# Kernel optimization log

Hardware: AMD Instinct MI355X
Metric: run time of the kernel (lower is better)

Reference implementation:

```python
import jax, jax.numpy as jnp
import numpy as np

HIDDEN = 256
NUM_STEPS = 3
N_NODES = 200000
N_GRAPHS = 512


def setup_inputs() -> dict:
    key = jax.random.key(0)
    ks = jax.random.split(key, 8)
    h = HIDDEN
    x = jax.random.normal(ks[0], (N_NODES, h), dtype=jnp.float32)
    batch = jnp.sort(jax.random.randint(ks[1], (N_NODES,), 0, N_GRAPHS)).astype(jnp.int64)
    s_ih = 1.0 / np.sqrt(2 * h)
    s_hh = 1.0 / np.sqrt(h)
    # LSTM (input 2h -> hidden h), PyTorch gate order i,f,g,o
    W_ih = jax.random.uniform(ks[2], (4 * h, 2 * h), jnp.float32, -s_ih, s_ih)
    W_hh = jax.random.uniform(ks[3], (4 * h, h), jnp.float32, -s_hh, s_hh)
    b_ih = jax.random.uniform(ks[4], (4 * h,), jnp.float32, -s_hh, s_hh)
    b_hh = jax.random.uniform(ks[5], (4 * h,), jnp.float32, -s_hh, s_hh)
    # out_proj: Linear(2h -> h)
    s_o = 1.0 / np.sqrt(2 * h)
    W_out = jax.random.uniform(ks[6], (h, 2 * h), jnp.float32, -s_o, s_o)
    b_out = jax.random.uniform(ks[7], (h,), jnp.float32, -s_o, s_o)
    return {"x": x, "batch": batch, "W_ih": W_ih, "W_hh": W_hh,
            "b_ih": b_ih, "b_hh": b_hh, "W_out": W_out, "b_out": b_out,
            "n_graphs": N_GRAPHS}


def _set2set(x, batch, W_ih, W_hh, b_ih, b_hh, n_graphs):
    h = x.shape[1]
    hs = jnp.zeros((n_graphs, h), x.dtype)
    cs = jnp.zeros((n_graphs, h), x.dtype)
    q_star = jnp.zeros((n_graphs, 2 * h), x.dtype)
    for _ in range(NUM_STEPS):
        # LSTM step (PyTorch gate order: i, f, g, o)
        gates = q_star @ W_ih.T + hs @ W_hh.T + (b_ih + b_hh)  # [B, 4h]
        i_g, f_g, g_g, o_g = jnp.split(gates, 4, axis=-1)
        cs = jax.nn.sigmoid(f_g) * cs + jax.nn.sigmoid(i_g) * jnp.tanh(g_g)
        hs = jax.nn.sigmoid(o_g) * jnp.tanh(cs)
        q = hs  # [B, h]
        # attention logits per node
        e = jnp.sum(x * q[batch], axis=-1)  # [N]
        # segment softmax over nodes of each graph
        m = jax.ops.segment_max(e, batch, num_segments=n_graphs)
        a = jnp.exp(e - m[batch])
        denom = jax.ops.segment_sum(a, batch, num_segments=n_graphs)
        a = a / denom[batch]
        # weighted readout
        r = jax.ops.segment_sum(a[:, None] * x, batch, num_segments=n_graphs)  # [B, h]
        q_star = jnp.concatenate([q, r], axis=-1)  # [B, 2h]
    return q_star


def reference(x, batch, W_ih, W_hh, b_ih, b_hh, W_out, b_out, n_graphs):
    q_star = _set2set(x, batch.astype(jnp.int32), W_ih, W_hh, b_ih, b_hh, n_graphs)
    return q_star @ W_out.T + b_out
```

## Files before the change

### kernel.cpp

```cpp
#include <hip/hip_runtime.h>
#include <hip/hip_bf16.h>

#define HID 256
#define NG 512
#define CHUNK 32

__device__ __forceinline__ float sigmoidf(float v) { return 1.f / (1.f + __expf(-v)); }

__device__ __forceinline__ void load_lds16(const void* g, void* l) {
    __builtin_amdgcn_global_load_lds(
        (const __attribute__((address_space(1))) void*)g,
        (__attribute__((address_space(3))) void*)l, 16, 0, 0);
}

__global__ __launch_bounds__(256) void prep_kernel(
    const float* __restrict__ W_ih, const float* __restrict__ W_hh,
    const float* __restrict__ b_ih, const float* __restrict__ b_hh,
    float* __restrict__ Wcat, float* __restrict__ bcat)
{
    int idx = blockIdx.x * 256 + threadIdx.x;
    if (idx < 1024 * 512) {
        int k = idx & 511;
        float v = W_ih[idx];
        if (k < 256) v += W_hh[(idx >> 9) * 256 + k];
        Wcat[idx] = v;
    }
    if (idx < 1024) bcat[idx] = b_ih[idx] + b_hh[idx];
}

__global__ __launch_bounds__(256) void find_starts(
    const int* __restrict__ batch, int n, int* __restrict__ starts)
{
    int g = blockIdx.x * 256 + threadIdx.x;
    if (g > NG) return;
    if (g == NG) { starts[NG] = n; return; }
    int lo = 0, hi = n;
    while (lo < hi) {
        int mid = (lo + hi) >> 1;
        if (batch[mid] < g) lo = mid + 1; else hi = mid;
    }
    starts[g] = lo;
}

__global__ __launch_bounds__(256) void lstm_cell(
    const float* __restrict__ gates, const float* __restrict__ bcat,
    float* __restrict__ cs, float* __restrict__ qs, int step0)
{
    int b = blockIdx.x, t = threadIdx.x;
    float ig, fg, gg, og, c_prev;
    if (step0) {
        ig = bcat[t]; fg = bcat[256 + t]; gg = bcat[512 + t]; og = bcat[768 + t];
        c_prev = 0.f;
    } else {
        const float* gr = gates + (size_t)b * 1024;
        ig = gr[t]; fg = gr[256 + t]; gg = gr[512 + t]; og = gr[768 + t];
        c_prev = cs[b * HID + t];
    }
    float c_new = sigmoidf(fg) * c_prev + sigmoidf(ig) * tanhf(gg);
    float h = sigmoidf(og) * tanhf(c_new);
    cs[b * HID + t] = c_new;
    qs[b * 512 + t] = h;
}

__global__ __launch_bounds__(256) void attention_kernel(
    const float* __restrict__ x, const int* __restrict__ starts,
    float* __restrict__ qs)
{
    __shared__ __align__(16) float xl[2][CHUNK * HID];
    __shared__ float ql[HID];
    __shared__ float e_arr[CHUNK];
    __shared__ float p_arr[CHUNK];
    __shared__ float m_s, s_s, a_s;

    const int g = blockIdx.x;
    const int tid = threadIdx.x;
    const int s0 = starts[g];
    const int nn = starts[g + 1] - s0;

    ql[tid] = qs[g * 512 + tid];
    if (tid == 0) { m_s = -3.402823466e38f; s_s = 0.f; a_s = 0.f; }
    float r_t = 0.f;
    __syncthreads();

    const int j = tid >> 3;
    const int s = tid & 7;
    const int lane = tid & 63;
    const int w = tid >> 6;

    float qreg[32];
    #pragma unroll
    for (int k = 0; k < 32; ++k) qreg[k] = ql[s + 8 * ((k + j) & 31)];

    if (nn > 0) {
        const char* src = (const char*)x + (size_t)s0 * (HID * 4);
        const int nchunks = (nn + CHUNK - 1) / CHUNK;

        {
            int bytes = (nn < CHUNK ? nn : CHUNK) * 1024;
            #pragma unroll
            for (int i = 0; i < 8; ++i) {
                int offw = i * 4096 + w * 1024;
                int offc = offw < bytes - 1024 ? offw : bytes - 1024;
                load_lds16(src + offc + lane * 16,
                           (char*)&xl[0][0] + offw + lane * 16);
            }
        }

        for (int c = 0; c < nchunks; ++c) {
            const int buf = c & 1;
            int rem = nn - c * CHUNK;
            const int nnc = rem < CHUNK ? rem : CHUNK;
            if (c + 1 < nchunks) {
                const char* src2 = src + (size_t)(c + 1) * (CHUNK * 1024);
                int rem2 = nn - (c + 1) * CHUNK;
                int bytes = (rem2 < CHUNK ? rem2 : CHUNK) * 1024;
                char* dst = (char*)&xl[buf ^ 1][0];
                #pragma unroll
                for (int i = 0; i < 8; ++i) {
                    int offw = i * 4096 + w * 1024;
                    int offc = offw < bytes - 1024 ? offw : bytes - 1024;
                    load_lds16(src2 + offc + lane * 16, dst + offw + lane * 16);
                }
                asm volatile("s_waitcnt vmcnt(8)" ::: "memory");
            } else {
                asm volatile("s_waitcnt vmcnt(0)" ::: "memory");
            }
            asm volatile("s_barrier" ::: "memory");

            const float* xb = &xl[buf][0];
            float acc = 0.f;
            #pragma unroll
            for (int k = 0; k < 32; ++k) {
                int col = s + 8 * ((k + j) & 31);
                acc += xb[j * HID + col] * qreg[k];
            }
            acc += __shfl_xor(acc, 1);
            acc += __shfl_xor(acc, 2);
            acc += __shfl_xor(acc, 4);
            if (s == 0) e_arr[j] = acc;
            asm volatile("s_waitcnt lgkmcnt(0)\n\ts_barrier" ::: "memory");

            if (tid < 64) {
                float e = (tid < nnc) ? e_arr[tid] : -3.402823466e38f;
                float cm = e;
                #pragma unroll
                for (int o = 32; o; o >>= 1) cm = fmaxf(cm, __shfl_xor(cm, o));
                float m_old = m_s;
                float m_new = fmaxf(m_old, cm);
                float al = __expf(m_old - m_new);
                float p = (tid < nnc) ? __expf(e - m_new) : 0.f;
                if (tid < CHUNK) p_arr[tid] = p;
                float ps = p;
                #pragma unroll
                for (int o = 32; o; o >>= 1) ps += __shfl_xor(ps, o);
                if (tid == 0) { s_s = s_s * al + ps; m_s = m_new; a_s = al; }
            }
            asm volatile("s_waitcnt lgkmcnt(0)\n\ts_barrier" ::: "memory");

            float al = a_s;
            r_t *= al;
            for (int jj = 0; jj < nnc; ++jj)
                r_t += p_arr[jj] * xb[jj * HID + tid];
            asm volatile("s_waitcnt lgkmcnt(0)\n\ts_barrier" ::: "memory");
        }
    }
    float denom = (nn > 0) ? s_s : 1.f;
    qs[g * 512 + HID + tid] = r_t / denom;
}

__global__ __launch_bounds__(256) void gemm_bias(
    const float* __restrict__ A, int lda,
    const float* __restrict__ B, int ldb,
    const float* __restrict__ bias,
    float* __restrict__ C, int ldc, int K)
{
    __shared__ float As[64][33];
    __shared__ float Bs[32][33];
    const int tid = threadIdx.x;
    const int m0 = blockIdx.y * 64;
    const int n0 = blockIdx.x * 32;
    const int tx = tid & 15, ty = tid >> 4;
    float acc[4][2] = {};

    for (int k0 = 0; k0 < K; k0 += 32) {
        #pragma unroll
        for (int i = 0; i < 2; ++i) {
            int idx = tid + i * 256;
            int r = idx >> 3, cc = (idx & 7) * 4;
            const float4 v = *(const float4*)&A[(size_t)(m0 + r) * lda + k0 + cc];
            As[r][cc] = v.x; As[r][cc + 1] = v.y; As[r][cc + 2] = v.z; As[r][cc + 3] = v.w;
        }
        {
            int r = tid >> 3, cc = (tid & 7) * 4;
            const float4 v = *(const float4*)&B[(size_t)(n0 + r) * ldb + k0 + cc];
            Bs[r][cc] = v.x; Bs[r][cc + 1] = v.y; Bs[r][cc + 2] = v.z; Bs[r][cc + 3] = v.w;
        }
        __syncthreads();
        #pragma unroll
        for (int kk = 0; kk < 32; ++kk) {
            float b0 = Bs[tx * 2][kk], b1 = Bs[tx * 2 + 1][kk];
            float a0 = As[ty * 4][kk],     a1 = As[ty * 4 + 1][kk];
            float a2 = As[ty * 4 + 2][kk], a3 = As[ty * 4 + 3][kk];
            acc[0][0] += a0 * b0; acc[0][1] += a0 * b1;
            acc[1][0] += a1 * b0; acc[1][1] += a1 * b1;
            acc[2][0] += a2 * b0; acc[2][1] += a2 * b1;
            acc[3][0] += a3 * b0; acc[3][1] += a3 * b1;
        }
        __syncthreads();
    }
    float bb0 = bias[n0 + tx * 2], bb1 = bias[n0 + tx * 2 + 1];
    #pragma unroll
    for (int i = 0; i < 4; ++i) {
        int row = m0 + ty * 4 + i;
        float* cr = &C[(size_t)row * ldc + n0 + tx * 2];
        cr[0] = acc[i][0] + bb0;
        cr[1] = acc[i][1] + bb1;
    }
}

extern "C" void kernel_launch(void* const* d_in, const int* in_sizes, int n_in,
                              void* d_out, int out_size, void* d_ws, size_t ws_size,
                              hipStream_t stream)
{
    const float* x     = (const float*)d_in[0];
    const int*   batch = (const int*)d_in[1];
    const float* W_ih  = (const float*)d_in[2];
    const float* W_hh  = (const float*)d_in[3];
    const float* b_ih  = (const float*)d_in[4];
    const float* b_hh  = (const float*)d_in[5];
    const float* W_out = (const float*)d_in[6];
    const float* b_out = (const float*)d_in[7];
    float* out = (float*)d_out;
    const int n = in_sizes[1];

    char* ws = (char*)d_ws;
    float* qs     = (float*)(ws);
    float* cs     = (float*)(ws + 1048576);
    float* gates  = (float*)(ws + 1572864);
    float* Wcat   = (float*)(ws + 3670016);
    float* bcat   = (float*)(ws + 5767168);
    int*   starts = (int*)  (ws + 5771264);

    prep_kernel<<<2048, 256, 0, stream>>>(W_ih, W_hh, b_ih, b_hh, Wcat, bcat);
    find_starts<<<3, 256, 0, stream>>>(batch, n, starts);

    for (int step = 0; step < 3; ++step) {
        if (step > 0) {
            gemm_bias<<<dim3(32, 8), 256, 0, stream>>>(qs, 512, Wcat, 512, bcat,
                                                       gates, 1024, 512);
        }
        lstm_cell<<<NG, 256, 0, stream>>>(gates, bcat, cs, qs, step == 0);
        attention_kernel<<<NG, 256, 0, stream>>>(x, starts, qs);
    }
    gemm_bias<<<dim3(8, 8), 256, 0, stream>>>(qs, 512, W_out, 512, b_out,
                                              out, 256, 512);
}
```

Measured before the change: 488.0 us.

## Fuse LSTM cell into attention kernel and use split-K GEMMs

Folds the LSTM cell into the attention kernel, which now sums the split-K gate partials and the bias itself, so each step drops one launch and one round trip through global memory. The attention inner loop is restructured: each thread holds its x row segment in float4 registers and does an online softmax per wave with a per-thread accumulator, replacing the serial per-column p*x loop and two of the barriers per chunk. A final cross-row reduction goes through LDS. The GEMMs become split-K kernels with 4x4 register tiles and register prefetch, plus a finalize kernel that sums the partials, trading extra partial-buffer traffic for more parallel blocks.

```diff
diff --git a/kernel.cpp b/kernel.cpp
--- a/kernel.cpp
+++ b/kernel.cpp
@@ -5,7 +5,7 @@
 #define NG 512
 #define CHUNK 32
 
-__device__ __forceinline__ float sigmoidf(float v) { return 1.f / (1.f + __expf(-v)); }
+__device__ __forceinline__ float sigmoidf_(float v) { return 1.f / (1.f + __expf(-v)); }
 
 __device__ __forceinline__ void load_lds16(const void* g, void* l) {
     __builtin_amdgcn_global_load_lds(
@@ -42,179 +42,202 @@
     starts[g] = lo;
 }
 
-__global__ __launch_bounds__(256) void lstm_cell(
-    const float* __restrict__ gates, const float* __restrict__ bcat,
-    float* __restrict__ cs, float* __restrict__ qs, int step0)
-{
-    int b = blockIdx.x, t = threadIdx.x;
-    float ig, fg, gg, og, c_prev;
-    if (step0) {
-        ig = bcat[t]; fg = bcat[256 + t]; gg = bcat[512 + t]; og = bcat[768 + t];
-        c_prev = 0.f;
-    } else {
-        const float* gr = gates + (size_t)b * 1024;
-        ig = gr[t]; fg = gr[256 + t]; gg = gr[512 + t]; og = gr[768 + t];
-        c_prev = cs[b * HID + t];
-    }
-    float c_new = sigmoidf(fg) * c_prev + sigmoidf(ig) * tanhf(gg);
-    float h = sigmoidf(og) * tanhf(c_new);
-    cs[b * HID + t] = c_new;
-    qs[b * 512 + t] = h;
-}
-
-__global__ __launch_bounds__(256) void attention_kernel(
+__global__ __launch_bounds__(256) void attn_kernel(
     const float* __restrict__ x, const int* __restrict__ starts,
-    float* __restrict__ qs)
+    const float* __restrict__ gp0, const float* __restrict__ gp1,
+    const float* __restrict__ bcat, float* __restrict__ cs,
+    float* __restrict__ qs, int step0)
 {
     __shared__ __align__(16) float xl[2][CHUNK * HID];
-    __shared__ float ql[HID];
+    __shared__ __align__(16) float ql[HID];
     __shared__ float e_arr[CHUNK];
-    __shared__ float p_arr[CHUNK];
-    __shared__ float m_s, s_s, a_s;
 
     const int g = blockIdx.x;
     const int tid = threadIdx.x;
+    const int lane = tid & 63;
+
+    float ig, fg, gg, og, cp;
+    if (step0) {
+        ig = bcat[tid]; fg = bcat[256 + tid]; gg = bcat[512 + tid]; og = bcat[768 + tid];
+        cp = 0.f;
+    } else {
+        const float* a0 = gp0 + (size_t)g * 1024;
+        const float* a1 = gp1 + (size_t)g * 1024;
+        ig = a0[tid]       + a1[tid]       + bcat[tid];
+        fg = a0[256 + tid] + a1[256 + tid] + bcat[256 + tid];
+        gg = a0[512 + tid] + a1[512 + tid] + bcat[512 + tid];
+        og = a0[768 + tid] + a1[768 + tid] + bcat[768 + tid];
+        cp = cs[g * HID + tid];
+    }
+    float cn = sigmoidf_(fg) * cp + sigmoidf_(ig) * tanhf(gg);
+    float h  = sigmoidf_(og) * tanhf(cn);
+    cs[g * HID + tid] = cn;
+    qs[(size_t)g * 512 + tid] = h;
+    ql[tid] = h;
+
     const int s0 = starts[g];
     const int nn = starts[g + 1] - s0;
-
-    ql[tid] = qs[g * 512 + tid];
-    if (tid == 0) { m_s = -3.402823466e38f; s_s = 0.f; a_s = 0.f; }
-    float r_t = 0.f;
-    __syncthreads();
+    if (nn <= 0) { qs[(size_t)g * 512 + HID + tid] = 0.f; return; }
 
     const int j = tid >> 3;
     const int s = tid & 7;
-    const int lane = tid & 63;
+    const int row = lane & 31;
     const int w = tid >> 6;
 
-    float qreg[32];
-    #pragma unroll
-    for (int k = 0; k < 32; ++k) qreg[k] = ql[s + 8 * ((k + j) & 31)];
-
-    if (nn > 0) {
-        const char* src = (const char*)x + (size_t)s0 * (HID * 4);
-        const int nchunks = (nn + CHUNK - 1) / CHUNK;
-
-        {
-            int bytes = (nn < CHUNK ? nn : CHUNK) * 1024;
+    const int nchunks = (nn + CHUNK - 1) / CHUNK;
+    const int tail = nn - (nchunks - 1) * CHUNK;
+
+    if (nchunks <= 2 && tail < CHUNK) {
+        float4 z = make_float4(0.f, 0.f, 0.f, 0.f);
+        int base = (nchunks - 1) & 1;
+        int cnt = (CHUNK - tail) * HID;
+        for (int off = tid * 4; off < cnt; off += 1024)
+            *(float4*)&xl[base][tail * HID + off] = z;
+    }
+
+    const char* src = (const char*)x + (size_t)s0 * 1024;
+
+    {
+        int bytes = (nn < CHUNK ? nn : CHUNK) * 1024;
+        #pragma unroll
+        for (int i = 0; i < 8; ++i) {
+            int offw = i * 4096 + w * 1024;
+            int offc = offw < bytes - 1024 ? offw : bytes - 1024;
+            load_lds16(src + offc + lane * 16, (char*)&xl[0][0] + offw + lane * 16);
+        }
+    }
+    asm volatile("s_waitcnt lgkmcnt(0)\n\ts_barrier" ::: "memory");
+
+    float4 qf[8];
+    #pragma unroll
+    for (int k = 0; k < 8; ++k) qf[k] = *(const float4*)&ql[k * 32 + s * 4];
+
+    float m_run = -3.402823466e38f, l_run = 0.f;
+    float4 racc[8] = {};
+
+    for (int c = 0; c < nchunks; ++c) {
+        const int buf = c & 1;
+        int rem = nn - c * CHUNK;
+        const int nnc = rem < CHUNK ? rem : CHUNK;
+        if (c + 1 < nchunks) {
+            const char* src2 = src + (size_t)(c + 1) * (CHUNK * 1024);
+            int rem2 = nn - (c + 1) * CHUNK;
+            int bytes = (rem2 < CHUNK ? rem2 : CHUNK) * 1024;
+            char* dst = (char*)&xl[buf ^ 1][0];
             #pragma unroll
             for (int i = 0; i < 8; ++i) {
                 int offw = i * 4096 + w * 1024;
                 int offc = offw < bytes - 1024 ? offw : bytes - 1024;
-                load_lds16(src + offc + lane * 16,
-                           (char*)&xl[0][0] + offw + lane * 16);
+                load_lds16(src2 + offc + lane * 16, dst + offw + lane * 16);
             }
-        }
-
-        for (int c = 0; c < nchunks; ++c) {
-            const int buf = c & 1;
-            int rem = nn - c * CHUNK;
-            const int nnc = rem < CHUNK ? rem : CHUNK;
-            if (c + 1 < nchunks) {
-                const char* src2 = src + (size_t)(c + 1) * (CHUNK * 1024);
-                int rem2 = nn - (c + 1) * CHUNK;
-                int bytes = (rem2 < CHUNK ? rem2 : CHUNK) * 1024;
-                char* dst = (char*)&xl[buf ^ 1][0];
-                #pragma unroll
-                for (int i = 0; i < 8; ++i) {
-                    int offw = i * 4096 + w * 1024;
-                    int offc = offw < bytes - 1024 ? offw : bytes - 1024;
-                    load_lds16(src2 + offc + lane * 16, dst + offw + lane * 16);
-                }
-                asm volatile("s_waitcnt vmcnt(8)" ::: "memory");
-            } else {
-                asm volatile("s_waitcnt vmcnt(0)" ::: "memory");
-            }
-            asm volatile("s_barrier" ::: "memory");
-
-            const float* xb = &xl[buf][0];
-            float acc = 0.f;
-            #pragma unroll
-            for (int k = 0; k < 32; ++k) {
-                int col = s + 8 * ((k + j) & 31);
-                acc += xb[j * HID + col] * qreg[k];
-            }
-            acc += __shfl_xor(acc, 1);
-            acc += __shfl_xor(acc, 2);
-            acc += __shfl_xor(acc, 4);
-            if (s == 0) e_arr[j] = acc;
-            asm volatile("s_waitcnt lgkmcnt(0)\n\ts_barrier" ::: "memory");
-
-            if (tid < 64) {
-                float e = (tid < nnc) ? e_arr[tid] : -3.402823466e38f;
-                float cm = e;
-                #pragma unroll
-                for (int o = 32; o; o >>= 1) cm = fmaxf(cm, __shfl_xor(cm, o));
-                float m_old = m_s;
-                float m_new = fmaxf(m_old, cm);
-                float al = __expf(m_old - m_new);
-                float p = (tid < nnc) ? __expf(e - m_new) : 0.f;
-                if (tid < CHUNK) p_arr[tid] = p;
-                float ps = p;
-                #pragma unroll
-                for (int o = 32; o; o >>= 1) ps += __shfl_xor(ps, o);
-                if (tid == 0) { s_s = s_s * al + ps; m_s = m_new; a_s = al; }
-            }
-            asm volatile("s_waitcnt lgkmcnt(0)\n\ts_barrier" ::: "memory");
-
-            float al = a_s;
-            r_t *= al;
-            for (int jj = 0; jj < nnc; ++jj)
-                r_t += p_arr[jj] * xb[jj * HID + tid];
-            asm volatile("s_waitcnt lgkmcnt(0)\n\ts_barrier" ::: "memory");
-        }
-    }
-    float denom = (nn > 0) ? s_s : 1.f;
-    qs[g * 512 + HID + tid] = r_t / denom;
-}
-
-__global__ __launch_bounds__(256) void gemm_bias(
+            asm volatile("s_waitcnt vmcnt(8)" ::: "memory");
+        } else {
+            asm volatile("s_waitcnt vmcnt(0)" ::: "memory");
+        }
+        asm volatile("s_barrier" ::: "memory");
+
+        const float* xb = &xl[buf][0];
+        float4 xr[8];
+        #pragma unroll
+        for (int k = 0; k < 8; ++k) xr[k] = *(const float4*)&xb[j * HID + k * 32 + s * 4];
+
+        float e = 0.f;
+        #pragma unroll
+        for (int k = 0; k < 8; ++k)
+            e += xr[k].x * qf[k].x + xr[k].y * qf[k].y + xr[k].z * qf[k].z + xr[k].w * qf[k].w;
+        e += __shfl_xor(e, 1); e += __shfl_xor(e, 2); e += __shfl_xor(e, 4);
+        if (s == 0) e_arr[j] = e;
+        asm volatile("s_waitcnt lgkmcnt(0)\n\ts_barrier" ::: "memory");
+
+        float eL = (row < nnc) ? e_arr[row] : -3.402823466e38f;
+        float mc = eL;
+        #pragma unroll
+        for (int o = 16; o; o >>= 1) mc = fmaxf(mc, __shfl_xor(mc, o));
+        float m_new = fmaxf(m_run, mc);
+        float alpha = __expf(m_run - m_new);
+        float pL = (row < nnc) ? __expf(eL - m_new) : 0.f;
+        float ps = pL;
+        #pragma unroll
+        for (int o = 16; o; o >>= 1) ps += __shfl_xor(ps, o);
+        l_run = l_run * alpha + ps;
+        m_run = m_new;
+        float p = __shfl(pL, j);
+
+        #pragma unroll
+        for (int k = 0; k < 8; ++k) {
+            racc[k].x = racc[k].x * alpha + p * xr[k].x;
+            racc[k].y = racc[k].y * alpha + p * xr[k].y;
+            racc[k].z = racc[k].z * alpha + p * xr[k].z;
+            racc[k].w = racc[k].w * alpha + p * xr[k].w;
+        }
+    }
+
+    asm volatile("s_waitcnt lgkmcnt(0)\n\ts_barrier" ::: "memory");
+    float* red = &xl[0][0];
+    #pragma unroll
+    for (int k = 0; k < 8; ++k)
+        *(float4*)&red[j * HID + k * 32 + s * 4] = racc[k];
+    asm volatile("s_waitcnt lgkmcnt(0)\n\ts_barrier" ::: "memory");
+    float sum = 0.f;
+    #pragma unroll
+    for (int jj = 0; jj < 32; ++jj) sum += red[jj * HID + tid];
+    qs[(size_t)g * 512 + HID + tid] = sum / l_run;
+}
+
+__global__ __launch_bounds__(256) void gemm_splitk(
     const float* __restrict__ A, int lda,
     const float* __restrict__ B, int ldb,
-    const float* __restrict__ bias,
-    float* __restrict__ C, int ldc, int K)
-{
-    __shared__ float As[64][33];
-    __shared__ float Bs[32][33];
+    float* __restrict__ Cp, int ldc, int KS, size_t slice_stride)
+{
+    __shared__ float As[16][76];
+    __shared__ float Bs[16][76];
     const int tid = threadIdx.x;
-    const int m0 = blockIdx.y * 64;
-    const int n0 = blockIdx.x * 32;
     const int tx = tid & 15, ty = tid >> 4;
-    float acc[4][2] = {};
-
-    for (int k0 = 0; k0 < K; k0 += 32) {
-        #pragma unroll
-        for (int i = 0; i < 2; ++i) {
-            int idx = tid + i * 256;
-            int r = idx >> 3, cc = (idx & 7) * 4;
-            const float4 v = *(const float4*)&A[(size_t)(m0 + r) * lda + k0 + cc];
-            As[r][cc] = v.x; As[r][cc + 1] = v.y; As[r][cc + 2] = v.z; As[r][cc + 3] = v.w;
-        }
-        {
-            int r = tid >> 3, cc = (tid & 7) * 4;
-            const float4 v = *(const float4*)&B[(size_t)(n0 + r) * ldb + k0 + cc];
-            Bs[r][cc] = v.x; Bs[r][cc + 1] = v.y; Bs[r][cc + 2] = v.z; Bs[r][cc + 3] = v.w;
-        }
+    const int m0 = blockIdx.y * 64, n0 = blockIdx.x * 64;
+    const int kb = blockIdx.z * KS;
+    const int r = tid >> 2, kc = (tid & 3) << 2;
+    float acc[4][4] = {};
+
+    const float* Ap = &A[(size_t)(m0 + r) * lda + kb + kc];
+    const float* Bp = &B[(size_t)(n0 + r) * ldb + kb + kc];
+    float4 av = *(const float4*)Ap;
+    float4 bv = *(const float4*)Bp;
+
+    for (int k0 = 0; k0 < KS; k0 += 16) {
+        As[kc + 0][r] = av.x; As[kc + 1][r] = av.y; As[kc + 2][r] = av.z; As[kc + 3][r] = av.w;
+        Bs[kc + 0][r] = bv.x; Bs[kc + 1][r] = bv.y; Bs[kc + 2][r] = bv.z; Bs[kc + 3][r] = bv.w;
         __syncthreads();
-        #pragma unroll
-        for (int kk = 0; kk < 32; ++kk) {
-            float b0 = Bs[tx * 2][kk], b1 = Bs[tx * 2 + 1][kk];
-            float a0 = As[ty * 4][kk],     a1 = As[ty * 4 + 1][kk];
-            float a2 = As[ty * 4 + 2][kk], a3 = As[ty * 4 + 3][kk];
-            acc[0][0] += a0 * b0; acc[0][1] += a0 * b1;
-            acc[1][0] += a1 * b0; acc[1][1] += a1 * b1;
-            acc[2][0] += a2 * b0; acc[2][1] += a2 * b1;
-            acc[3][0] += a3 * b0; acc[3][1] += a3 * b1;
+        if (k0 + 16 < KS) {
+            av = *(const float4*)(Ap + k0 + 16);
+            bv = *(const float4*)(Bp + k0 + 16);
+        }
+        #pragma unroll
+        for (int kk = 0; kk < 16; ++kk) {
+            float4 a = *(const float4*)&As[kk][ty << 2];
+            float4 b = *(const float4*)&Bs[kk][tx << 2];
+            acc[0][0] += a.x * b.x; acc[0][1] += a.x * b.y; acc[0][2] += a.x * b.z; acc[0][3] += a.x * b.w;
+            acc[1][0] += a.y * b.x; acc[1][1] += a.y * b.y; acc[1][2] += a.y * b.z; acc[1][3] += a.y * b.w;
+            acc[2][0] += a.z * b.x; acc[2][1] += a.z * b.y; acc[2][2] += a.z * b.z; acc[2][3] += a.z * b.w;
+            acc[3][0] += a.w * b.x; acc[3][1] += a.w * b.y; acc[3][2] += a.w * b.z; acc[3][3] += a.w * b.w;
         }
         __syncthreads();
     }
-    float bb0 = bias[n0 + tx * 2], bb1 = bias[n0 + tx * 2 + 1];
+    float* out = Cp + blockIdx.z * slice_stride;
     #pragma unroll
     for (int i = 0; i < 4; ++i) {
-        int row = m0 + ty * 4 + i;
-        float* cr = &C[(size_t)row * ldc + n0 + tx * 2];
-        cr[0] = acc[i][0] + bb0;
-        cr[1] = acc[i][1] + bb1;
+        float4 o = make_float4(acc[i][0], acc[i][1], acc[i][2], acc[i][3]);
+        *(float4*)&out[(size_t)(m0 + ty * 4 + i) * ldc + n0 + (tx << 2)] = o;
+    }
+}
+
+__global__ __launch_bounds__(256) void finalize_out(
+    const float* __restrict__ op, const float* __restrict__ b_out,
+    float* __restrict__ out)
+{
+    int i = blockIdx.x * 256 + threadIdx.x;
+    if (i < 512 * 256) {
+        float v = op[i] + op[131072 + i] + op[262144 + i] + op[393216 + i] + b_out[i & 255];
+        out[i] = v;
     }
 }
 
@@ -232,26 +255,29 @@
     const float* b_out = (const float*)d_in[7];
     float* out = (float*)d_out;
     const int n = in_sizes[1];
+    (void)n_in; (void)out_size; (void)ws_size;
 
     char* ws = (char*)d_ws;
-    float* qs     = (float*)(ws);
-    float* cs     = (float*)(ws + 1048576);
-    float* gates  = (float*)(ws + 1572864);
-    float* Wcat   = (float*)(ws + 3670016);
-    float* bcat   = (float*)(ws + 5767168);
-    int*   starts = (int*)  (ws + 5771264);
+    float* qs      = (float*)(ws);
+    float* cs      = (float*)(ws + 0x100000);
+    float* gates_p = (float*)(ws + 0x180000);
+    float* Wcat    = (float*)(ws + 0x580000);
+    float* bcat    = (float*)(ws + 0x780000);
+    int*   starts  = (int*)  (ws + 0x781000);
+    float* out_p   = (float*)(ws + 0x790000);
 
     prep_kernel<<<2048, 256, 0, stream>>>(W_ih, W_hh, b_ih, b_hh, Wcat, bcat);
     find_starts<<<3, 256, 0, stream>>>(batch, n, starts);
 
     for (int step = 0; step < 3; ++step) {
         if (step > 0) {
-            gemm_bias<<<dim3(32, 8), 256, 0, stream>>>(qs, 512, Wcat, 512, bcat,
-                                                       gates, 1024, 512);
-        }
-        lstm_cell<<<NG, 256, 0, stream>>>(gates, bcat, cs, qs, step == 0);
-        attention_kernel<<<NG, 256, 0, stream>>>(x, starts, qs);
-    }
-    gemm_bias<<<dim3(8, 8), 256, 0, stream>>>(qs, 512, W_out, 512, b_out,
-                                              out, 256, 512);
-}
+            gemm_splitk<<<dim3(16, 8, 2), 256, 0, stream>>>(
+                qs, 512, Wcat, 512, gates_p, 1024, 256, (size_t)512 * 1024);
+        }
+        attn_kernel<<<NG, 256, 0, stream>>>(
+            x, starts, gates_p, gates_p + (size_t)512 * 1024, bcat, cs, qs, step == 0);
+    }
+    gemm_splitk<<<dim3(4, 8, 4), 256, 0, stream>>>(
+        qs, 512, W_out, 512, out_p, 256, 128, (size_t)512 * 256);
+    finalize_out<<<512, 256, 0, stream>>>(out_p, b_out, out);
+}
```

Result: faster. 420.3 us (-13.9%).
